# Performance work log

Measured on AMD Instinct MI355X. Metric: run time of the kernel, lower is better.

Reference implementation:

```python
import jax, jax.numpy as jnp
import numpy as np

B, N, D, H = 2, 2048, 1024, 16
HD = D // H  # 64
EPS = 1e-6


def setup_inputs() -> dict:
    key = jax.random.key(0)
    ks = jax.random.split(key, 16)
    rnd = lambda k, shp: jax.random.normal(k, shp, dtype=jnp.float32)
    w = lambda k, i, o: rnd(k, (i, o)) * 0.02  # stored as (in, out); y = x @ W
    return {
        "x": rnd(ks[0], (B, N, D)),
        "emb_B_D": rnd(ks[1], (B, D)),
        "gate": rnd(ks[2], (B, D)),
        "crossattn_emb": rnd(ks[3], (B, 128, D)),
        "rope_emb_L_1_1_D": rnd(ks[4], (N, HD)),
        "Wq1": w(ks[5], D, D), "Wq2": w(ks[6], D, D),
        "Wk1": w(ks[7], D, D), "Wk2": w(ks[8], D, D),
        "Wv": w(ks[9], D, D),
        "Wo": w(ks[10], D, D),
        "Wada1": w(ks[11], D, D),
        "Wada2": w(ks[12], D, 2 * D),
        "bada2": jnp.zeros((2 * D,), dtype=jnp.float32),
    }


def rotate_half(t):
    t1, t2 = jnp.split(t, 2, axis=-1)
    return jnp.concatenate([-t2, t1], axis=-1)


def reference(x, emb_B_D, gate, crossattn_emb, rope_emb_L_1_1_D,
              Wq1, Wq2, Wk1, Wk2, Wv, Wo, Wada1, Wada2, bada2):
    # adaLN modulation: SiLU -> Linear(no bias) -> Linear(bias)
    ada = jax.nn.silu(emb_B_D) @ Wada1 @ Wada2 + bada2          # [B, 2D]
    shift, scale = jnp.split(ada, 2, axis=1)                    # [B, D] each

    # LayerNorm (no affine) + scale/shift
    mu = jnp.mean(x, axis=-1, keepdims=True)
    var = jnp.var(x, axis=-1, keepdims=True)
    xn = (x - mu) * jax.lax.rsqrt(var + EPS)
    xn = xn * (1.0 + scale[:, None, :]) + shift[:, None, :]     # [B, N, D]

    # QKV projections (each to_q/to_k is two stacked linears, to_v one)
    q = xn @ Wq1 @ Wq2
    k = xn @ Wk1 @ Wk2
    v = xn @ Wv
    split_heads = lambda t: t.reshape(B, N, H, HD).transpose(0, 2, 1, 3)  # b h n d
    q, k, v = split_heads(q), split_heads(k), split_heads(v)

    # RoPE
    cos = jnp.cos(rope_emb_L_1_1_D)[None, None]                 # [1,1,N,HD]
    sin = jnp.sin(rope_emb_L_1_1_D)[None, None]
    q = q * cos + rotate_half(q) * sin
    k = k * cos + rotate_half(k) * sin

    # Attention
    sim = jnp.einsum("bhid,bhjd->bhij", q, k) * (HD ** -0.5)
    attn = jax.nn.softmax(sim, axis=-1)
    out = jnp.einsum("bhij,bhjd->bhid", attn, v)
    out = out.transpose(0, 2, 1, 3).reshape(B, N, D) @ Wo

    # Gated residual
    return x + gate[:, None, :] * out
```

## Files before the change

kernel.cpp:

```cpp
#include <hip/hip_runtime.h>
#include <stdint.h>
#include <math.h>

typedef unsigned short u16;
typedef __attribute__((ext_vector_type(8))) short short8;
typedef __attribute__((ext_vector_type(4))) float f32x4;
typedef __attribute__((ext_vector_type(4))) unsigned short u16x4;
typedef __attribute__((ext_vector_type(2))) unsigned int uint2v;

#define DEV static __device__ __forceinline__

DEV u16 f2bf(float f) {
    unsigned u = __builtin_bit_cast(unsigned, f);
    u = u + 0x7fffu + ((u >> 16) & 1u);
    return (u16)(u >> 16);
}
DEV float bf2f(u16 s) { return __builtin_bit_cast(float, ((unsigned)s) << 16); }
DEV unsigned pk2(float a, float b) {
    unsigned ua = __builtin_bit_cast(unsigned, a) + 0x8000u;
    unsigned ub = __builtin_bit_cast(unsigned, b) + 0x8000u;
    return (ua >> 16) | (ub & 0xffff0000u);
}
DEV float fexp2(float x) {
#if __has_builtin(__builtin_amdgcn_exp2f)
    return __builtin_amdgcn_exp2f(x);
#else
    return __expf(x * 0.69314718056f);
#endif
}

DEV void gl_lds16(const u16* g, u16* l) {
#if __has_builtin(__builtin_amdgcn_global_load_lds)
    __builtin_amdgcn_global_load_lds((const __attribute__((address_space(1))) unsigned int*)g,
                                     (__attribute__((address_space(3))) unsigned int*)l, 16, 0, 0);
#else
    *(short8*)l = *(const short8*)g;
#endif
}


__global__ __launch_bounds__(256) void k_ada1(const float* __restrict__ emb, const float* __restrict__ W,
                                              float* __restrict__ out) {
    int col = blockIdx.x * 64 + (threadIdx.x & 63);
    int b = blockIdx.y;
    int kseg = threadIdx.x >> 6;
    float acc = 0.f;
    for (int k = kseg * 256; k < kseg * 256 + 256; k++) {
        float e = emb[b * 1024 + k];
        float se = e / (1.f + __expf(-e));
        acc += se * W[(size_t)k * 1024 + col];
    }
    __shared__ float red[4][64];
    red[kseg][threadIdx.x & 63] = acc;
    __syncthreads();
    if (threadIdx.x < 64)
        out[b * 1024 + blockIdx.x * 64 + threadIdx.x] =
            red[0][threadIdx.x] + red[1][threadIdx.x] + red[2][threadIdx.x] + red[3][threadIdx.x];
}

__global__ __launch_bounds__(256) void k_prep(const float* s0, u16* d0, const float* s1, u16* d1,
                                              const float* s2, u16* d2, const float* s3, u16* d3,
                                              const float* s4, u16* d4, const float* s5, u16* d5,
                                              const float* __restrict__ t_ada, const float* __restrict__ Wada2,
                                              const float* __restrict__ bada2, float* __restrict__ ada,
                                              const float* __restrict__ rope,
                                              float* __restrict__ cst, float* __restrict__ snt) {
    __shared__ u16 tile[64][65];
    __shared__ float red[4][64];
    if (blockIdx.z == 6) {
        int flat = blockIdx.y * 16 + blockIdx.x;
        if (flat < 64) {
            int b = flat >> 5, xb = flat & 31;
            int col = xb * 64 + (threadIdx.x & 63);
            int kseg = threadIdx.x >> 6;
            float acc = 0.f;
            for (int k = kseg * 256; k < kseg * 256 + 256; k++)
                acc += t_ada[b * 1024 + k] * Wada2[(size_t)k * 2048 + col];
            red[kseg][threadIdx.x & 63] = acc;
            __syncthreads();
            if (threadIdx.x < 64) {
                int c = xb * 64 + threadIdx.x;
                ada[b * 2048 + c] = red[0][threadIdx.x] + red[1][threadIdx.x] +
                                    red[2][threadIdx.x] + red[3][threadIdx.x] + bada2[c];
            }
        } else if (flat < 192) {
            int idx = (flat - 64) * 1024 + threadIdx.x * 4;
            float4 rv = *(const float4*)(rope + idx);
            float4 cv, sv;
            __sincosf(rv.x, &sv.x, &cv.x);
            __sincosf(rv.y, &sv.y, &cv.y);
            __sincosf(rv.z, &sv.z, &cv.z);
            __sincosf(rv.w, &sv.w, &cv.w);
            *(float4*)(cst + idx) = cv;
            *(float4*)(snt + idx) = sv;
        }
        return;
    }
    const float* s; u16* d;
    switch (blockIdx.z) {
        case 0: s = s0; d = d0; break;
        case 1: s = s1; d = d1; break;
        case 2: s = s2; d = d2; break;
        case 3: s = s3; d = d3; break;
        case 4: s = s4; d = d4; break;
        default: s = s5; d = d5; break;
    }
    int k0 = blockIdx.x * 64, n0 = blockIdx.y * 64;
    int tx = threadIdx.x & 63, ty = threadIdx.x >> 6;
    if (blockIdx.z >= 4) {
        #pragma unroll
        for (int i = 0; i < 16; i++) {
            int kk = ty + 4 * i;
            d[(size_t)(k0 + kk) * 1024 + n0 + tx] = f2bf(s[(size_t)(k0 + kk) * 1024 + n0 + tx]);
        }
        return;
    }
    #pragma unroll
    for (int i = 0; i < 16; i++) {
        int kk = ty + 4 * i;
        tile[kk][tx] = f2bf(s[(size_t)(k0 + kk) * 1024 + n0 + tx]);
    }
    __syncthreads();
    #pragma unroll
    for (int i = 0; i < 16; i++) {
        int nn = ty + 4 * i;
        d[(size_t)(n0 + nn) * 1024 + k0 + tx] = tile[tx][nn];
    }
}

__global__ __launch_bounds__(256) void k_ln(const float* __restrict__ x, const float* __restrict__ ada,
                                            u16* __restrict__ xn) {
    int row = blockIdx.x;
    int b = row >> 11;
    float4 v = ((const float4*)(x + (size_t)row * 1024))[threadIdx.x];
    float s = v.x + v.y + v.z + v.w;
    float ss = v.x * v.x + v.y * v.y + v.z * v.z + v.w * v.w;
    #pragma unroll
    for (int m = 1; m < 64; m <<= 1) { s += __shfl_xor(s, m, 64); ss += __shfl_xor(ss, m, 64); }
    __shared__ float red[2][4];
    int wave = threadIdx.x >> 6, lane = threadIdx.x & 63;
    if (lane == 0) { red[0][wave] = s; red[1][wave] = ss; }
    __syncthreads();
    s = red[0][0] + red[0][1] + red[0][2] + red[0][3];
    ss = red[1][0] + red[1][1] + red[1][2] + red[1][3];
    float mu = s * (1.f / 1024.f);
    float var = ss * (1.f / 1024.f) - mu * mu;
    float rs = rsqrtf(var + 1e-6f);
    int c = threadIdx.x * 4;
    const float* sh = ada + b * 2048;
    const float* sc = ada + b * 2048 + 1024;
    u16x4 r;
    r.x = f2bf((v.x - mu) * rs * (1.f + sc[c + 0]) + sh[c + 0]);
    r.y = f2bf((v.y - mu) * rs * (1.f + sc[c + 1]) + sh[c + 1]);
    r.z = f2bf((v.z - mu) * rs * (1.f + sc[c + 2]) + sh[c + 2]);
    r.w = f2bf((v.w - mu) * rs * (1.f + sc[c + 3]) + sh[c + 3]);
    *(u16x4*)(xn + (size_t)row * 1024 + c) = r;
}

template <int BM, int BN, int MODE>
DEV void gemm_core(const u16* __restrict__ A, const u16* __restrict__ Bt,
                   u16* __restrict__ Cb, float* __restrict__ Cf, u16* __restrict__ Vt,
                   const float* __restrict__ Xres, const float* __restrict__ gate,
                   const float* __restrict__ cst, const float* __restrict__ snt,
                   float scale, int Nn, int K, int m0, int n0) {
    constexpr int MI = BM / 32, NJ = BN / 32;
    __shared__ u16 As[BM][64];
    __shared__ u16 Bs[BN][64];
    int tid = threadIdx.x;
    int lane = tid & 63, wave = tid >> 6;
    int wm = (wave & 1) * (BM / 2), wn = (wave >> 1) * (BN / 2);
    int lr = lane & 15, quad = lane >> 4;
    f32x4 acc[MI][NJ];
    #pragma unroll
    for (int i = 0; i < MI; i++)
        #pragma unroll
        for (int j = 0; j < NJ; j++) acc[i][j] = f32x4{0.f, 0.f, 0.f, 0.f};

    int arow = tid >> 3;
    int acol = (tid & 7) * 8;
    int g8 = (((tid & 7) ^ (arow & 7))) * 8;
    int cc[2] = { ((quad ^ (lr & 7))) * 8, (((4 + quad) ^ (lr & 7))) * 8 };

    for (int k0 = 0; k0 < K; k0 += 64) {
        #pragma unroll
        for (int p = 0; p < MI; p++)
            gl_lds16(A + (size_t)(m0 + arow + 32 * p) * K + k0 + g8, &As[arow + 32 * p][acol]);
        #pragma unroll
        for (int p = 0; p < NJ; p++)
            gl_lds16(Bt + (size_t)(n0 + arow + 32 * p) * K + k0 + g8, &Bs[arow + 32 * p][acol]);
        __syncthreads();
        #pragma unroll
        for (int ks = 0; ks < 2; ks++) {
            short8 af[MI], bfr[NJ];
            #pragma unroll
            for (int i = 0; i < MI; i++) af[i] = *(const short8*)(&As[wm + i * 16 + lr][cc[ks]]);
            #pragma unroll
            for (int j = 0; j < NJ; j++) bfr[j] = *(const short8*)(&Bs[wn + j * 16 + lr][cc[ks]]);
            #pragma unroll
            for (int i = 0; i < MI; i++)
                #pragma unroll
                for (int j = 0; j < NJ; j++)
                    acc[i][j] = __builtin_amdgcn_mfma_f32_16x16x32_bf16(af[i], bfr[j], acc[i][j], 0, 0, 0);
        }
        __syncthreads();
    }

    if (MODE == 2) {
        if ((n0 + wn) < 2048) {
            #pragma unroll
            for (int i = 0; i < MI; i++)
                #pragma unroll
                for (int jp = 0; jp < 2; jp++)
                    #pragma unroll
                    for (int r = 0; r < 4; r++) {
                        int row = m0 + wm + i * 16 + quad * 4 + r;
                        int n = row & 2047;
                        int d1 = jp * 16 + lr;
                        float c1 = cst[n * 64 + d1],      s1 = snt[n * 64 + d1];
                        float c2 = cst[n * 64 + d1 + 32], s2 = snt[n * 64 + d1 + 32];
                        float x1 = acc[i][jp][r], x2 = acc[i][jp + 2][r];
                        Cb[(size_t)row * Nn + n0 + wn + d1]      = f2bf(x1 * c1 - x2 * s1);
                        Cb[(size_t)row * Nn + n0 + wn + d1 + 32] = f2bf(x2 * c2 + x1 * s2);
                    }
        } else {
            int hv = (n0 + wn - 2048) >> 6;
            #pragma unroll
            for (int i = 0; i < MI; i++)
                #pragma unroll
                for (int j = 0; j < NJ; j++) {
                    int token = m0 + wm + i * 16 + quad * 4;
                    int bb = token >> 11;
                    int nloc = token & 2047;
                    u16x4 w;
                    w.x = f2bf(acc[i][j][0]); w.y = f2bf(acc[i][j][1]);
                    w.z = f2bf(acc[i][j][2]); w.w = f2bf(acc[i][j][3]);
                    *(u16x4*)(Vt + ((size_t)((bb * 16 + hv) * 64 + j * 16 + lr)) * 2048 + nloc) = w;
                }
        }
        return;
    }
    #pragma unroll
    for (int i = 0; i < MI; i++)
        #pragma unroll
        for (int j = 0; j < NJ; j++)
            #pragma unroll
            for (int r = 0; r < 4; r++) {
                int row = m0 + wm + i * 16 + quad * 4 + r;
                int col = n0 + wn + j * 16 + lr;
                float v = acc[i][j][r];
                if (MODE == 1) {
                    int b = row >> 11;
                    Cf[(size_t)row * Nn + col] = Xres[(size_t)row * Nn + col] + gate[b * 1024 + col] * v;
                } else {
                    Cb[(size_t)row * Nn + col] = f2bf(v * scale);
                }
            }
}

template <int BM, int BN, int MODE>
__global__ __launch_bounds__(256) void gemm_bt(const u16* __restrict__ A, const u16* __restrict__ Bt,
                                               u16* __restrict__ Cb, float* __restrict__ Cf,
                                               u16* __restrict__ Vt,
                                               const float* __restrict__ Xres, const float* __restrict__ gate,
                                               const float* __restrict__ cst, const float* __restrict__ snt,
                                               int Nn, int K) {
    gemm_core<BM, BN, MODE>(A, Bt, Cb, Cf, Vt, Xres, gate, cst, snt, 1.f, Nn, K,
                            blockIdx.y * BM, blockIdx.x * BN);
}

__global__ __launch_bounds__(256) void gemm_fold(const u16* A0, const u16* B0, u16* C0,
                                                 const u16* A1, const u16* B1, u16* C1) {
    const u16* A = blockIdx.z ? A1 : A0;
    const u16* Bt = blockIdx.z ? B1 : B0;
    u16* C = blockIdx.z ? C1 : C0;
    float scale = blockIdx.z ? 1.0f : 0.18033688f;
    gemm_core<64, 64, 0>(A, Bt, C, nullptr, nullptr, nullptr, nullptr, nullptr, nullptr, scale,
                         1024, 1024, blockIdx.y * 64, blockIdx.x * 64);
}

__global__ __launch_bounds__(256) void k_attn(const u16* __restrict__ qkv, const u16* __restrict__ vt,
                                              u16* __restrict__ dump, float* __restrict__ paL) {
    __shared__ u16 pool[128 * 72];
    __shared__ u16 Ks[2][64][64];
    __shared__ u16 Vs[2][64][64];
    int q0 = blockIdx.x * 128;
    int bh = blockIdx.y; int b = bh >> 4, h = bh & 15;
    int z = blockIdx.z;
    int kbase = z * 1024;
    int tid = threadIdx.x;
    int lane = tid & 63, wave = tid >> 6;
    int lr = lane & 15, quad = lane >> 4;
    int srow = tid >> 3, scol = (tid & 7) * 8;
    int sg = (((tid & 7) ^ (srow & 7))) * 8;
    int cc[2] = { ((quad ^ (lr & 7))) * 8, (((4 + quad) ^ (lr & 7))) * 8 };

    const u16* kp = qkv + ((size_t)(b * 2048 + kbase + srow)) * 2048 + 1024 + h * 64 + sg;
    const u16* vp = vt + ((size_t)(bh * 64 + srow)) * 2048 + kbase + sg;

    #pragma unroll
    for (int p = 0; p < 4; p++)
        gl_lds16(qkv + ((size_t)(b * 2048 + q0 + srow + 32 * p)) * 2048 + h * 64 + sg,
                 pool + (srow + 32 * p) * 64 + scol);

    short8 krA[2], vrA[2], krB[2], vrB[2];
    krA[0] = *(const short8*)(kp);               krA[1] = *(const short8*)(kp + (size_t)32 * 2048);
    vrA[0] = *(const short8*)(vp);               vrA[1] = *(const short8*)(vp + (size_t)32 * 2048);
    __syncthreads();
    short8 qf[2][2];
    #pragma unroll
    for (int rt = 0; rt < 2; rt++)
        #pragma unroll
        for (int ks = 0; ks < 2; ks++)
            qf[rt][ks] = *(const short8*)(pool + (wave * 32 + rt * 16 + lr) * 64 + cc[ks]);
    *(short8*)(&Ks[0][srow][scol])      = krA[0];
    *(short8*)(&Ks[0][srow + 32][scol]) = krA[1];
    *(short8*)(&Vs[0][srow][scol])      = vrA[0];
    *(short8*)(&Vs[0][srow + 32][scol]) = vrA[1];
    krB[0] = *(const short8*)(kp + (size_t)64 * 2048);  krB[1] = *(const short8*)(kp + (size_t)96 * 2048);
    vrB[0] = *(const short8*)(vp + 64);                 vrB[1] = *(const short8*)(vp + 64 + (size_t)32 * 2048);
    __syncthreads();

    float l_part[2] = {0.f, 0.f};
    f32x4 oacc[2][4];
    #pragma unroll
    for (int rt = 0; rt < 2; rt++)
        #pragma unroll
        for (int dt = 0; dt < 4; dt++) oacc[rt][dt] = f32x4{0.f, 0.f, 0.f, 0.f};

    auto body = [&](int it, int cur, short8 (&krF)[2], short8 (&vrF)[2],
                    short8 (&krH)[2], short8 (&vrH)[2]) {
        if (it < 14) {
            const u16* kq = kp + (size_t)(it + 2) * 64 * 2048;
            const u16* vq = vp + (it + 2) * 64;
            krF[0] = *(const short8*)(kq);  krF[1] = *(const short8*)(kq + (size_t)32 * 2048);
            vrF[0] = *(const short8*)(vq);  vrF[1] = *(const short8*)(vq + (size_t)32 * 2048);
        }
        f32x4 st[2][4];
        #pragma unroll
        for (int rt = 0; rt < 2; rt++)
            #pragma unroll
            for (int ct = 0; ct < 4; ct++) st[rt][ct] = f32x4{0.f, 0.f, 0.f, 0.f};
        #pragma unroll
        for (int ks = 0; ks < 2; ks++) {
            short8 kf[4];
            #pragma unroll
            for (int ct = 0; ct < 4; ct++)
                kf[ct] = *(const short8*)(&Ks[cur][ct * 16 + lr][cc[ks]]);
            #pragma unroll
            for (int rt = 0; rt < 2; rt++)
                #pragma unroll
                for (int ct = 0; ct < 4; ct++)
                    st[rt][ct] = __builtin_amdgcn_mfma_f32_16x16x32_bf16(kf[ct], qf[rt][ks], st[rt][ct], 0, 0, 0);
        }
        #pragma unroll
        for (int rt = 0; rt < 2; rt++)
            #pragma unroll
            for (int ct = 0; ct < 4; ct++) {
                float p0 = fexp2(st[rt][ct][0]);
                float p1 = fexp2(st[rt][ct][1]);
                float p2 = fexp2(st[rt][ct][2]);
                float p3 = fexp2(st[rt][ct][3]);
                l_part[rt] += (p0 + p1) + (p2 + p3);
                uint2v w; w.x = pk2(p0, p1); w.y = pk2(p2, p3);
                *(uint2v*)(pool + (wave * 32 + rt * 16 + lr) * 72 + ct * 16 + quad * 4) = w;
            }
        #pragma unroll
        for (int ks = 0; ks < 2; ks++) {
            short8 pf[2], vf[4];
            #pragma unroll
            for (int rt = 0; rt < 2; rt++)
                pf[rt] = *(const short8*)(pool + (wave * 32 + rt * 16 + lr) * 72 + ks * 32 + quad * 8);
            #pragma unroll
            for (int dt = 0; dt < 4; dt++)
                vf[dt] = *(const short8*)(&Vs[cur][dt * 16 + lr][cc[ks]]);
            #pragma unroll
            for (int rt = 0; rt < 2; rt++)
                #pragma unroll
                for (int dt = 0; dt < 4; dt++)
                    oacc[rt][dt] = __builtin_amdgcn_mfma_f32_16x16x32_bf16(pf[rt], vf[dt], oacc[rt][dt], 0, 0, 0);
        }
        if (it < 15) {
            int nxt = cur ^ 1;
            *(short8*)(&Ks[nxt][srow][scol])      = krH[0];
            *(short8*)(&Ks[nxt][srow + 32][scol]) = krH[1];
            *(short8*)(&Vs[nxt][srow][scol])      = vrH[0];
            *(short8*)(&Vs[nxt][srow + 32][scol]) = vrH[1];
        }
        __syncthreads();
    };

    #pragma unroll 1
    for (int it2 = 0; it2 < 8; ++it2) {
        body(2 * it2,     0, krA, vrA, krB, vrB);
        body(2 * it2 + 1, 1, krB, vrB, krA, vrA);
    }

    #pragma unroll
    for (int rt = 0; rt < 2; rt++) {
        float l = l_part[rt];
        l += __shfl_xor(l, 16, 64);
        l += __shfl_xor(l, 32, 64);
        if (quad == 0)
            paL[(size_t)z * 65536 + bh * 2048 + q0 + wave * 32 + rt * 16 + lr] = l;
    }
    u16* dp = dump + (size_t)z * 4194304 + ((size_t)(bh * 16 + blockIdx.x) * 256 + tid) * 32;
    #pragma unroll
    for (int rt = 0; rt < 2; rt++)
        #pragma unroll
        for (int dt = 0; dt < 4; dt++) {
            u16x4 w;
            w.x = f2bf(oacc[rt][dt][0]); w.y = f2bf(oacc[rt][dt][1]);
            w.z = f2bf(oacc[rt][dt][2]); w.w = f2bf(oacc[rt][dt][3]);
            *(u16x4*)(dp + rt * 16 + dt * 4) = w;
        }
}

__global__ __launch_bounds__(256) void k_comb(const u16* __restrict__ dump, const float* __restrict__ paL,
                                              u16* __restrict__ aob) {
    int bx = blockIdx.x, bh = blockIdx.y;
    int b = bh >> 4, h = bh & 15;
    int tid = threadIdx.x;
    int lane = tid & 63, wave = tid >> 6;
    int lr = lane & 15, quad = lane >> 4;
    int q0 = bx * 128;
    const u16* d0 = dump + ((size_t)(bh * 16 + bx) * 256 + tid) * 32;
    const u16* d1 = d0 + 4194304;
    #pragma unroll
    for (int rt = 0; rt < 2; rt++) {
        float inv[4];
        #pragma unroll
        for (int r = 0; r < 4; r++) {
            int row = q0 + wave * 32 + rt * 16 + quad * 4 + r;
            float l0 = paL[bh * 2048 + row];
            float l1 = paL[65536 + bh * 2048 + row];
            inv[r] = 1.f / (l0 + l1);
        }
        #pragma unroll
        for (int dt = 0; dt < 4; dt++) {
            u16x4 w0 = *(const u16x4*)(d0 + rt * 16 + dt * 4);
            u16x4 w1 = *(const u16x4*)(d1 + rt * 16 + dt * 4);
            #pragma unroll
            for (int r = 0; r < 4; r++) {
                int row = q0 + wave * 32 + rt * 16 + quad * 4 + r;
                float o = (bf2f(((const u16*)&w0)[r]) + bf2f(((const u16*)&w1)[r])) * inv[r];
                aob[((size_t)(b * 2048 + row)) * 1024 + h * 64 + dt * 16 + lr] = f2bf(o);
            }
        }
    }
}

extern "C" void kernel_launch(void* const* d_in, const int* in_sizes, int n_in,
                              void* d_out, int out_size, void* d_ws, size_t ws_size,
                              hipStream_t stream) {
    const float* x     = (const float*)d_in[0];
    const float* emb   = (const float*)d_in[1];
    const float* gate  = (const float*)d_in[2];
    const float* rope  = (const float*)d_in[4];
    const float* Wq1   = (const float*)d_in[5];
    const float* Wq2   = (const float*)d_in[6];
    const float* Wk1   = (const float*)d_in[7];
    const float* Wk2   = (const float*)d_in[8];
    const float* Wv    = (const float*)d_in[9];
    const float* Wo    = (const float*)d_in[10];
    const float* Wada1 = (const float*)d_in[11];
    const float* Wada2 = (const float*)d_in[12];
    const float* bada2 = (const float*)d_in[13];
    float* out = (float*)d_out;

    char* ws = (char*)d_ws;
    size_t off = 0;
    auto alloc = [&](size_t bytes) { void* p = ws + off; off += (bytes + 255) & ~(size_t)255; return p; };
    float* t_ada = (float*)alloc(2048 * 4);
    float* ada   = (float*)alloc(4096 * 4);
    float* cst   = (float*)alloc((size_t)131072 * 4);
    float* snt   = (float*)alloc((size_t)131072 * 4);
    u16* xn    = (u16*)alloc((size_t)4096 * 1024 * 2);
    u16* Wq1b  = (u16*)alloc((size_t)1024 * 1024 * 2);
    u16* Wk1b  = (u16*)alloc((size_t)1024 * 1024 * 2);
    u16* Wq2t  = (u16*)alloc((size_t)1024 * 1024 * 2);
    u16* Wk2t  = (u16*)alloc((size_t)1024 * 1024 * 2);
    u16* Wot   = (u16*)alloc((size_t)1024 * 1024 * 2);
    u16* WqkvT = (u16*)alloc((size_t)3072 * 1024 * 2);
    u16* qkvb  = (u16*)alloc((size_t)4096 * 2048 * 2);
    u16* vtb   = (u16*)alloc((size_t)4096 * 1024 * 2);
    u16* aob   = (u16*)alloc((size_t)4096 * 1024 * 2);
    u16* dumpO = (u16*)alloc((size_t)2 * 4194304 * 2);
    float* paL = (float*)alloc((size_t)2 * 65536 * 4);
    (void)ws_size; (void)in_sizes; (void)n_in; (void)out_size;

    k_ada1<<<dim3(16, 2), 256, 0, stream>>>(emb, Wada1, t_ada);

    k_prep<<<dim3(16, 16, 7), 256, 0, stream>>>(Wq2, Wq2t, Wk2, Wk2t,
                                                Wv, WqkvT + (size_t)2048 * 1024, Wo, Wot,
                                                Wq1, Wq1b, Wk1, Wk1b,
                                                t_ada, Wada2, bada2, ada, rope, cst, snt);

    k_ln<<<4096, 256, 0, stream>>>(x, ada, xn);

    gemm_fold<<<dim3(16, 16, 2), 256, 0, stream>>>(Wq2t, Wq1b, WqkvT,
                                                   Wk2t, Wk1b, WqkvT + (size_t)1024 * 1024);

    gemm_bt<128, 128, 2><<<dim3(24, 32), 256, 0, stream>>>(xn, WqkvT, qkvb, nullptr, vtb,
                                                           nullptr, nullptr, cst, snt, 2048, 1024);

    k_attn<<<dim3(16, 32, 2), 256, 0, stream>>>(qkvb, vtb, dumpO, paL);
    k_comb<<<dim3(16, 32), 256, 0, stream>>>(dumpO, paL, aob);

    gemm_bt<128, 64, 1><<<dim3(16, 32), 256, 0, stream>>>(aob, Wot, nullptr, out, nullptr, x, gate,
                                                          nullptr, nullptr, 1024, 1024);
}
```

Before: 293.4 us.

## Double-buffer GEMM LDS tiles with register prefetch and set occupancy hints

Replaces the direct global-to-LDS load plus two barriers per K step with a register-staged prefetch two iterations ahead and double-buffered LDS, leaving one barrier per step. Global-load latency is meant to overlap the MFMA work on the current tile. Launch bounds now carry waves-per-EU hints for each GEMM. The loop hardcodes K=1024 (16 iterations), and the doubled LDS plus extra registers may lower occupancy.

```diff
diff --git a/kernel.cpp b/kernel.cpp
--- a/kernel.cpp
+++ b/kernel.cpp
@@ -164,8 +164,8 @@
                    const float* __restrict__ cst, const float* __restrict__ snt,
                    float scale, int Nn, int K, int m0, int n0) {
     constexpr int MI = BM / 32, NJ = BN / 32;
-    __shared__ u16 As[BM][64];
-    __shared__ u16 Bs[BN][64];
+    __shared__ u16 As[2][BM][64];
+    __shared__ u16 Bs[2][BN][64];
     int tid = threadIdx.x;
     int lane = tid & 63, wave = tid >> 6;
     int wm = (wave & 1) * (BM / 2), wn = (wave >> 1) * (BN / 2);
@@ -181,28 +181,59 @@
     int g8 = (((tid & 7) ^ (arow & 7))) * 8;
     int cc[2] = { ((quad ^ (lr & 7))) * 8, (((4 + quad) ^ (lr & 7))) * 8 };
 
-    for (int k0 = 0; k0 < K; k0 += 64) {
-        #pragma unroll
-        for (int p = 0; p < MI; p++)
-            gl_lds16(A + (size_t)(m0 + arow + 32 * p) * K + k0 + g8, &As[arow + 32 * p][acol]);
-        #pragma unroll
-        for (int p = 0; p < NJ; p++)
-            gl_lds16(Bt + (size_t)(n0 + arow + 32 * p) * K + k0 + g8, &Bs[arow + 32 * p][acol]);
-        __syncthreads();
+    const u16* ap = A + (size_t)(m0 + arow) * K + g8;
+    const u16* bp = Bt + (size_t)(n0 + arow) * K + g8;
+
+    short8 ra[2][MI], rb[2][NJ];
+    #pragma unroll
+    for (int p = 0; p < MI; p++) ra[0][p] = *(const short8*)(ap + (size_t)(32 * p) * K);
+    #pragma unroll
+    for (int p = 0; p < NJ; p++) rb[0][p] = *(const short8*)(bp + (size_t)(32 * p) * K);
+    #pragma unroll
+    for (int p = 0; p < MI; p++) *(short8*)(&As[0][arow + 32 * p][acol]) = ra[0][p];
+    #pragma unroll
+    for (int p = 0; p < NJ; p++) *(short8*)(&Bs[0][arow + 32 * p][acol]) = rb[0][p];
+    #pragma unroll
+    for (int p = 0; p < MI; p++) ra[1][p] = *(const short8*)(ap + 64 + (size_t)(32 * p) * K);
+    #pragma unroll
+    for (int p = 0; p < NJ; p++) rb[1][p] = *(const short8*)(bp + 64 + (size_t)(32 * p) * K);
+    __syncthreads();
+
+    auto body = [&](int it, int cur) {
+        if (it + 2 < 16) {
+            const u16* aq = ap + (size_t)(it + 2) * 64;
+            const u16* bq = bp + (size_t)(it + 2) * 64;
+            #pragma unroll
+            for (int p = 0; p < MI; p++) ra[cur][p] = *(const short8*)(aq + (size_t)(32 * p) * K);
+            #pragma unroll
+            for (int p = 0; p < NJ; p++) rb[cur][p] = *(const short8*)(bq + (size_t)(32 * p) * K);
+        }
         #pragma unroll
         for (int ks = 0; ks < 2; ks++) {
             short8 af[MI], bfr[NJ];
             #pragma unroll
-            for (int i = 0; i < MI; i++) af[i] = *(const short8*)(&As[wm + i * 16 + lr][cc[ks]]);
-            #pragma unroll
-            for (int j = 0; j < NJ; j++) bfr[j] = *(const short8*)(&Bs[wn + j * 16 + lr][cc[ks]]);
+            for (int i = 0; i < MI; i++) af[i] = *(const short8*)(&As[cur][wm + i * 16 + lr][cc[ks]]);
+            #pragma unroll
+            for (int j = 0; j < NJ; j++) bfr[j] = *(const short8*)(&Bs[cur][wn + j * 16 + lr][cc[ks]]);
             #pragma unroll
             for (int i = 0; i < MI; i++)
                 #pragma unroll
                 for (int j = 0; j < NJ; j++)
                     acc[i][j] = __builtin_amdgcn_mfma_f32_16x16x32_bf16(af[i], bfr[j], acc[i][j], 0, 0, 0);
         }
+        if (it + 1 < 16) {
+            int nxt = cur ^ 1;
+            #pragma unroll
+            for (int p = 0; p < MI; p++) *(short8*)(&As[nxt][arow + 32 * p][acol]) = ra[nxt][p];
+            #pragma unroll
+            for (int p = 0; p < NJ; p++) *(short8*)(&Bs[nxt][arow + 32 * p][acol]) = rb[nxt][p];
+        }
         __syncthreads();
+    };
+    #pragma unroll 1
+    for (int it2 = 0; it2 < 8; ++it2) {
+        body(2 * it2, 0);
+        body(2 * it2 + 1, 1);
     }
 
     if (MODE == 2) {
@@ -257,19 +288,19 @@
             }
 }
 
-template <int BM, int BN, int MODE>
-__global__ __launch_bounds__(256) void gemm_bt(const u16* __restrict__ A, const u16* __restrict__ Bt,
-                                               u16* __restrict__ Cb, float* __restrict__ Cf,
-                                               u16* __restrict__ Vt,
-                                               const float* __restrict__ Xres, const float* __restrict__ gate,
-                                               const float* __restrict__ cst, const float* __restrict__ snt,
-                                               int Nn, int K) {
+template <int BM, int BN, int MODE, int WPE>
+__global__ __launch_bounds__(256, WPE) void gemm_bt(const u16* __restrict__ A, const u16* __restrict__ Bt,
+                                                    u16* __restrict__ Cb, float* __restrict__ Cf,
+                                                    u16* __restrict__ Vt,
+                                                    const float* __restrict__ Xres, const float* __restrict__ gate,
+                                                    const float* __restrict__ cst, const float* __restrict__ snt,
+                                                    int Nn, int K) {
     gemm_core<BM, BN, MODE>(A, Bt, Cb, Cf, Vt, Xres, gate, cst, snt, 1.f, Nn, K,
                             blockIdx.y * BM, blockIdx.x * BN);
 }
 
-__global__ __launch_bounds__(256) void gemm_fold(const u16* A0, const u16* B0, u16* C0,
-                                                 const u16* A1, const u16* B1, u16* C1) {
+__global__ __launch_bounds__(256, 4) void gemm_fold(const u16* A0, const u16* B0, u16* C0,
+                                                    const u16* A1, const u16* B1, u16* C1) {
     const u16* A = blockIdx.z ? A1 : A0;
     const u16* Bt = blockIdx.z ? B1 : B0;
     u16* C = blockIdx.z ? C1 : C0;
@@ -500,12 +531,12 @@
     gemm_fold<<<dim3(16, 16, 2), 256, 0, stream>>>(Wq2t, Wq1b, WqkvT,
                                                    Wk2t, Wk1b, WqkvT + (size_t)1024 * 1024);
 
-    gemm_bt<128, 128, 2><<<dim3(24, 32), 256, 0, stream>>>(xn, WqkvT, qkvb, nullptr, vtb,
-                                                           nullptr, nullptr, cst, snt, 2048, 1024);
+    gemm_bt<128, 128, 2, 2><<<dim3(24, 32), 256, 0, stream>>>(xn, WqkvT, qkvb, nullptr, vtb,
+                                                              nullptr, nullptr, cst, snt, 2048, 1024);
 
     k_attn<<<dim3(16, 32, 2), 256, 0, stream>>>(qkvb, vtb, dumpO, paL);
     k_comb<<<dim3(16, 32), 256, 0, stream>>>(dumpO, paL, aob);
 
-    gemm_bt<128, 64, 1><<<dim3(16, 32), 256, 0, stream>>>(aob, Wot, nullptr, out, nullptr, x, gate,
-                                                          nullptr, nullptr, 1024, 1024);
-}
+    gemm_bt<128, 64, 1, 3><<<dim3(16, 32), 256, 0, stream>>>(aob, Wot, nullptr, out, nullptr, x, gate,
+                                                             nullptr, nullptr, 1024, 1024);
+}
```

Result: faster. 279.8 us (-4.6%).
